# Kernel optimization log

Hardware: AMD Instinct MI355X
Metric: run time of the kernel (lower is better)

Reference implementation:

```python
import jax, jax.numpy as jnp
import numpy as np

D_MODEL = 1024
D_INNER = 2048
D_STATE = 16
D_CONV = 4
DT_RANK = 64
BATCH = 2
SEQ = 1024


def _silu(v):
    return v * jax.nn.sigmoid(v)


def setup_inputs() -> dict:
    key = jax.random.key(0)
    ks = jax.random.split(key, 8)
    s = 0.02
    return {
        "x": jax.random.normal(ks[0], (BATCH, SEQ, D_MODEL), jnp.float32),
        "norm_w": jnp.ones((D_MODEL,), jnp.float32),
        "in_proj_w": (jax.random.normal(ks[1], (2 * D_INNER, D_MODEL), jnp.float32) * s),
        "conv_w": (jax.random.normal(ks[2], (D_INNER, 1, D_CONV), jnp.float32) * s),
        "conv_b": jnp.zeros((D_INNER,), jnp.float32),
        "x_proj_w": (jax.random.normal(ks[3], (DT_RANK + 2 * D_STATE, D_INNER), jnp.float32) * s),
        "dt_proj_w": (jax.random.normal(ks[4], (D_INNER, DT_RANK), jnp.float32) * s),
        "dt_proj_b": jnp.zeros((D_INNER,), jnp.float32),
        "A_log": jnp.log(jnp.broadcast_to(jnp.arange(1, D_STATE + 1, dtype=jnp.float32), (D_INNER, D_STATE))),
        "D": jnp.ones((D_INNER,), jnp.float32),
        "out_proj_w": (jax.random.normal(ks[5], (D_MODEL, D_INNER), jnp.float32) * s),
    }


def reference(x, norm_w, in_proj_w, conv_w, conv_b, x_proj_w, dt_proj_w, dt_proj_b, A_log, D, out_proj_w):
    b, l, d = x.shape
    x_copy = x
    # MambaRMSNorm
    h = x * jax.lax.rsqrt(jnp.mean(x * x, axis=-1, keepdims=True) + 1e-5) * norm_w
    # in_proj -> split into x-path and residual gate
    x_and_res = h @ in_proj_w.T                       # [b, l, 2*d_inner]
    xs, res = jnp.split(x_and_res, 2, axis=-1)
    # causal depthwise conv1d (torch pads d_conv-1 both sides then slices [:l])
    xc = jnp.transpose(xs, (0, 2, 1))                 # [b, d_inner, l]
    xc = jax.lax.conv_general_dilated(
        xc, conv_w, window_strides=(1,), padding=[(D_CONV - 1, 0)],
        feature_group_count=D_INNER, dimension_numbers=("NCH", "OIH", "NCH"))
    xc = xc + conv_b[None, :, None]
    u = _silu(jnp.transpose(xc, (0, 2, 1)))           # [b, l, d_inner]
    # SSM parameters
    A = -jnp.exp(A_log)                               # [d_inner, n]
    x_dbl = u @ x_proj_w.T                            # [b, l, dt_rank + 2n]
    delta, Bm, Cm = jnp.split(x_dbl, [DT_RANK, DT_RANK + D_STATE], axis=-1)
    delta = jax.nn.softplus(delta @ dt_proj_w.T + dt_proj_b)   # [b, l, d_inner]
    deltaA = jnp.exp(jnp.einsum("bld,dn->bldn", delta, A))     # [b, l, d_inner, n]
    deltaB_u = (delta * u)[..., None] * Bm[:, :, None, :]      # [b, l, d_inner, n]

    def step(state, inp):
        dA, dBu, c = inp                               # [b,d,n],[b,d,n],[b,n]
        state = dA * state + dBu
        y = jnp.einsum("bdn,bn->bd", state, c)
        return state, y

    init = jnp.zeros((b, D_INNER, D_STATE), dtype=u.dtype)
    _, ys = jax.lax.scan(
        step, init,
        (jnp.transpose(deltaA, (1, 0, 2, 3)),
         jnp.transpose(deltaB_u, (1, 0, 2, 3)),
         jnp.transpose(Cm, (1, 0, 2))))
    y = jnp.transpose(ys, (1, 0, 2)) + u * D           # [b, l, d_inner]
    y = y * _silu(res)
    return y @ out_proj_w.T + x_copy
```

## Files before the change

### kernel.cpp

```cpp
#include <hip/hip_runtime.h>
#include <hip/hip_bf16.h>
#include <math.h>

constexpr int B_   = 2;
constexpr int L_   = 1024;
constexpr int DM   = 1024;
constexpr int DI   = 2048;
constexpr int NS   = 16;
constexpr int DTR  = 64;
constexpr int TOK  = B_ * L_;
constexpr int NC   = 32;

typedef __attribute__((ext_vector_type(8))) short short8;
typedef __attribute__((ext_vector_type(4))) float f32x4;
using bf16 = __hip_bfloat16;

__device__ __forceinline__ float sigmoidf_(float v) {
    return 1.f / (1.f + __expf(-v));
}
__device__ __forceinline__ float softplusf_(float v) {
    return fmaxf(v, 0.f) + __logf(1.f + __expf(-fabsf(v)));
}

__device__ __forceinline__ f32x4 mfma16(short8 a, short8 b, f32x4 c) {
    return __builtin_amdgcn_mfma_f32_16x16x32_bf16(a, b, c, 0, 0, 0);
}

__global__ __launch_bounds__(256) void k_rmsnorm(
    const float* __restrict__ x, const float* __restrict__ w,
    bf16* __restrict__ hh, bf16* __restrict__ hl)
{
    int row = blockIdx.x;
    const float4* xrp = (const float4*)(x + (size_t)row * DM);
    float4 v = xrp[threadIdx.x];
    float ss = v.x*v.x + v.y*v.y + v.z*v.z + v.w*v.w;
    #pragma unroll
    for (int m = 32; m >= 1; m >>= 1) ss += __shfl_xor(ss, m);
    __shared__ float acc[4];
    int wid = threadIdx.x >> 6, lane = threadIdx.x & 63;
    if (lane == 0) acc[wid] = ss;
    __syncthreads();
    float tot = acc[0] + acc[1] + acc[2] + acc[3];
    float sc = rsqrtf(tot * (1.f / DM) + 1e-5f);
    float4 wv = ((const float4*)w)[threadIdx.x];
    float o[4] = { v.x*sc*wv.x, v.y*sc*wv.y, v.z*sc*wv.z, v.w*sc*wv.w };
    alignas(8) bf16 H[4], Lo[4];
    #pragma unroll
    for (int j = 0; j < 4; ++j) {
        H[j]  = __float2bfloat16(o[j]);
        Lo[j] = __float2bfloat16(o[j] - __bfloat162float(H[j]));
    }
    size_t base = (size_t)row * DM + threadIdx.x * 4;
    *(ushort4*)(hh + base) = *(ushort4*)H;
    *(ushort4*)(hl + base) = *(ushort4*)Lo;
}

__global__ __launch_bounds__(256) void k_split(
    const float* __restrict__ s, bf16* __restrict__ hi, bf16* __restrict__ lo, int n4)
{
    int i = blockIdx.x * 256 + threadIdx.x;
    if (i >= n4) return;
    float4 v = ((const float4*)s)[i];
    float f[4] = { v.x, v.y, v.z, v.w };
    alignas(8) bf16 H[4], Lo[4];
    #pragma unroll
    for (int j = 0; j < 4; ++j) {
        H[j]  = __float2bfloat16(f[j]);
        Lo[j] = __float2bfloat16(f[j] - __bfloat162float(H[j]));
    }
    *(ushort4*)(hi + (size_t)i * 4) = *(ushort4*)H;
    *(ushort4*)(lo + (size_t)i * 4) = *(ushort4*)Lo;
}

__global__ __launch_bounds__(256) void k_split_pad(
    const float* __restrict__ s, bf16* __restrict__ hi, bf16* __restrict__ lo)
{
    int i = blockIdx.x * 256 + threadIdx.x;
    int row = i >> 9;
    float f[4] = {0.f, 0.f, 0.f, 0.f};
    if (row < 96) {
        float4 v = ((const float4*)s)[i];
        f[0] = v.x; f[1] = v.y; f[2] = v.z; f[3] = v.w;
    }
    alignas(8) bf16 H[4], Lo[4];
    #pragma unroll
    for (int j = 0; j < 4; ++j) {
        H[j]  = __float2bfloat16(f[j]);
        Lo[j] = __float2bfloat16(f[j] - __bfloat162float(H[j]));
    }
    *(ushort4*)(hi + (size_t)i * 4) = *(ushort4*)H;
    *(ushort4*)(lo + (size_t)i * 4) = *(ushort4*)Lo;
}

__global__ __launch_bounds__(256) void k_transpose(
    const float* __restrict__ in, float* __restrict__ out)
{
    __shared__ float tile[32][33];
    int tx = threadIdx.x & 31, ty = threadIdx.x >> 5;
    int c0 = blockIdx.x * 32, r0 = blockIdx.y * 32;
    #pragma unroll
    for (int i = 0; i < 4; ++i)
        tile[ty * 4 + i][tx] = in[(size_t)(r0 + ty * 4 + i) * DI + c0 + tx];
    __syncthreads();
    #pragma unroll
    for (int i = 0; i < 4; ++i)
        out[(size_t)(c0 + ty * 4 + i) * TOK + r0 + tx] = tile[tx][ty * 4 + i];
}

__global__ __launch_bounds__(256) void k_tr_bc(
    const float* __restrict__ xdbl, float* __restrict__ bc_t)
{
    int id = blockIdx.x * 256 + threadIdx.x;
    int tok = id & (TOK - 1);
    int j = id >> 11;
    bc_t[(size_t)j * TOK + tok] = xdbl[(size_t)tok * 96 + 64 + j];
}

__device__ __forceinline__ void stage_tile(const bf16* src, int ld, bf16* lds, int lane)
{
    #pragma unroll
    for (int j = 0; j < 8; ++j) {
        int c = (j << 6) + lane;
        int r = c >> 2;
        int g = (c & 3) ^ ((r >> 1) & 3);
        __builtin_amdgcn_global_load_lds(
            (const __attribute__((address_space(1))) unsigned int*)(src + (size_t)r * ld + (g << 3)),
            (__attribute__((address_space(3))) unsigned int*)(lds + (j << 9)),
            16, 0, 0);
    }
}

template<int NA, int EPI>
__global__ __launch_bounds__(256) void k_gemm_bf16(
    const bf16* __restrict__ Ah, const bf16* __restrict__ Al, int lda,
    const bf16* __restrict__ Bh, const bf16* __restrict__ Bl, int ldb,
    float* __restrict__ C, int ldc,
    const float* __restrict__ aux,
    int M, int Nb, int Kc)
{
    __shared__ alignas(1024) bf16 sA[2][NA][128 * 32];
    __shared__ alignas(1024) bf16 sB[2][2][128 * 32];

    int tid = threadIdx.x, lane = tid & 63, wv = tid >> 6;
    int bm0 = blockIdx.y * 128, bn0 = blockIdx.x * 128;
    int kbase = blockIdx.z * Kc;
    int nkt = Kc >> 5;

    const bf16* Abase_h = Ah + (size_t)bm0 * lda + kbase;
    const bf16* Abase_l = (NA == 2) ? (Al + (size_t)bm0 * lda + kbase) : nullptr;
    const bf16* Bbase_h = Bh + (size_t)bn0 * ldb + kbase;
    const bf16* Bbase_l = Bl + (size_t)bn0 * ldb + kbase;

    auto stage_all = [&](int buf, int kt) {
        int k0 = kt << 5;
        if constexpr (NA == 2) {
            if      (wv == 0) stage_tile(Abase_h + k0, lda, &sA[buf][0][0], lane);
            else if (wv == 1) stage_tile(Abase_l + k0, lda, &sA[buf][1][0], lane);
            else if (wv == 2) stage_tile(Bbase_h + k0, ldb, &sB[buf][0][0], lane);
            else              stage_tile(Bbase_l + k0, ldb, &sB[buf][1][0], lane);
        } else {
            if      (wv == 0) stage_tile(Abase_h + k0, lda, &sA[buf][0][0], lane);
            else if (wv == 1) stage_tile(Bbase_h + k0, ldb, &sB[buf][0][0], lane);
            else if (wv == 2) stage_tile(Bbase_l + k0, ldb, &sB[buf][1][0], lane);
        }
    };
    auto frag = [&](const bf16* t, int r, int g) -> short8 {
        int c = (r << 2) + (g ^ ((r >> 1) & 3));
        return *(const short8*)(t + (c << 3));
    };

    int wr = (wv >> 1) << 6;
    int wc = (wv & 1) << 6;
    int fr = lane & 15, g = lane >> 4;

    f32x4 acc[4][4] = {};

    stage_all(0, 0);
    __syncthreads();
    for (int kt = 0; kt < nkt; ++kt) {
        int cur = kt & 1;
        if (kt + 1 < nkt) stage_all(cur ^ 1, kt + 1);
        short8 a0[4], a1[4], b0[4], b1[4];
        #pragma unroll
        for (int m = 0; m < 4; ++m) {
            a0[m] = frag(&sA[cur][0][0], wr + m * 16 + fr, g);
            if constexpr (NA == 2) a1[m] = frag(&sA[cur][NA - 1][0], wr + m * 16 + fr, g);
        }
        #pragma unroll
        for (int n = 0; n < 4; ++n) {
            b0[n] = frag(&sB[cur][0][0], wc + n * 16 + fr, g);
            b1[n] = frag(&sB[cur][1][0], wc + n * 16 + fr, g);
        }
        #pragma unroll
        for (int m = 0; m < 4; ++m)
            #pragma unroll
            for (int n = 0; n < 4; ++n) {
                acc[m][n] = mfma16(a0[m], b0[n], acc[m][n]);
                acc[m][n] = mfma16(a0[m], b1[n], acc[m][n]);
                if constexpr (NA == 2) acc[m][n] = mfma16(a1[m], b0[n], acc[m][n]);
            }
        __syncthreads();
    }

    int rbase = bm0 + wr + (g << 2);
    int cb = bn0 + wc + fr;
    if constexpr (EPI == 4) {
        #pragma unroll
        for (int m = 0; m < 4; ++m)
            #pragma unroll
            for (int n = 0; n < 4; ++n) {
                int col = cb + n * 16;
                float b_ = aux[col];
                float vv[4];
                #pragma unroll
                for (int i = 0; i < 4; ++i)
                    vv[i] = softplusf_(acc[m][n][i] + b_);
                *(float4*)&C[(size_t)col * ldc + rbase + m * 16] = *(float4*)vv;
            }
    } else {
        #pragma unroll
        for (int m = 0; m < 4; ++m)
            #pragma unroll
            for (int i = 0; i < 4; ++i) {
                int row = rbase + m * 16 + i;
                #pragma unroll
                for (int n = 0; n < 4; ++n) {
                    int col = cb + n * 16;
                    float v = acc[m][n][i];
                    if constexpr (EPI == 3) {
                        if (col < Nb) atomicAdd(&C[(size_t)row * ldc + col], v);
                    } else {
                        if constexpr (EPI == 1) v = softplusf_(v + aux[col]);
                        if constexpr (EPI == 2) v += aux[(size_t)row * ldc + col];
                        C[(size_t)row * ldc + col] = v;
                    }
                }
            }
    }
}

__global__ __launch_bounds__(256) void k_conv_silu(
    const float* __restrict__ xr, const float* __restrict__ w,
    const float* __restrict__ bconv, float* __restrict__ u,
    bf16* __restrict__ uh, bf16* __restrict__ ul)
{
    int idx = blockIdx.x * 256 + threadIdx.x;
    int dq = idx & 511;
    int l  = (idx >> 9) & 1023;
    int bb = idx >> 19;
    int dd = dq * 4;

    float4 wrow[4];
    #pragma unroll
    for (int j = 0; j < 4; j++)
        wrow[j] = *(const float4*)&w[(dd + j) * 4];
    float4 bias4 = *(const float4*)&bconv[dd];

    float acc[4] = { bias4.x, bias4.y, bias4.z, bias4.w };
    #pragma unroll
    for (int k = 0; k < 4; k++) {
        int lp = l - 3 + k;
        if (lp >= 0) {
            const float4 xv = *(const float4*)
                &xr[((size_t)(bb * L_ + lp)) * (2 * DI) + dd];
            const float xs_[4] = { xv.x, xv.y, xv.z, xv.w };
            #pragma unroll
            for (int j = 0; j < 4; j++)
                acc[j] = fmaf(xs_[j], ((const float*)&wrow[j])[k], acc[j]);
        }
    }
    float out[4];
    alignas(8) bf16 H[4], Lo[4];
    #pragma unroll
    for (int j = 0; j < 4; j++) {
        out[j] = acc[j] * sigmoidf_(acc[j]);
        H[j]  = __float2bfloat16(out[j]);
        Lo[j] = __float2bfloat16(out[j] - __bfloat162float(H[j]));
    }
    size_t base = ((size_t)(bb * L_ + l)) * DI + dd;
    *(float4*)&u[base] = *(float4*)out;
    *(ushort4*)(uh + base) = *(ushort4*)H;
    *(ushort4*)(ul + base) = *(ushort4*)Lo;
}

__global__ __launch_bounds__(256) void k_scan_part(
    const float* __restrict__ delta_t, const float* __restrict__ u_t,
    const float* __restrict__ bc_t,    const float* __restrict__ A_log,
    float* __restrict__ P, float* __restrict__ S)
{
    int bx = blockIdx.x;
    int c = bx & (NC - 1);
    int rest = bx >> 5;
    int b = rest >> 5;
    int d0 = (rest & 31) << 6;
    int t = threadIdx.x;
    int dl_ = t >> 2, q = t & 3;
    int d = d0 + dl_;

    float A_dn[4];
    #pragma unroll
    for (int j = 0; j < 4; ++j)
        A_dn[j] = -__expf(A_log[d * NS + q * 4 + j]);

    float s[4] = {};
    float dsum = 0.f;
    int tokb = b * L_ + c * (L_ / NC);
    const float* dbase = delta_t + (size_t)d * TOK + tokb;
    const float* ubase = u_t + (size_t)d * TOK + tokb;
    const float* Bbase = bc_t + (size_t)(q * 4) * TOK + tokb;

    for (int g = 0; g < (L_ / NC) / 4; ++g) {
        float4 dl4 = *(const float4*)(dbase + g * 4);
        float4 uu4 = *(const float4*)(ubase + g * 4);
        float Bm_[4][4];
        #pragma unroll
        for (int j = 0; j < 4; ++j) {
            float4 bv = *(const float4*)(Bbase + (size_t)j * TOK + g * 4);
            Bm_[j][0] = bv.x; Bm_[j][1] = bv.y; Bm_[j][2] = bv.z; Bm_[j][3] = bv.w;
        }
        const float dls[4] = {dl4.x, dl4.y, dl4.z, dl4.w};
        const float uus[4] = {uu4.x, uu4.y, uu4.z, uu4.w};
        #pragma unroll
        for (int k = 0; k < 4; ++k) {
            float dlu = dls[k] * uus[k];
            dsum += dls[k];
            #pragma unroll
            for (int j = 0; j < 4; ++j) {
                float e = __expf(dls[k] * A_dn[j]);
                s[j] = fmaf(e, s[j], dlu * Bm_[j][k]);
            }
        }
    }
    float p[4];
    #pragma unroll
    for (int j = 0; j < 4; ++j)
        p[j] = __expf(A_dn[j] * dsum);
    size_t o = (((size_t)(b * NC + c) * DI) + d) * NS + q * 4;
    *(float4*)&P[o] = *(float4*)p;
    *(float4*)&S[o] = *(float4*)s;
}

__global__ __launch_bounds__(256) void k_scan_comb(
    const float* __restrict__ P, float* __restrict__ S)
{
    int idx = blockIdx.x * 256 + threadIdx.x;
    int n = idx & 15;
    int d = (idx >> 4) & (DI - 1);
    int b = idx >> 15;
    float carry = 0.f;
    #pragma unroll
    for (int c = 0; c < NC; ++c) {
        size_t o = (((size_t)(b * NC + c) * DI) + d) * NS + n;
        float Pv = P[o], Sv = S[o];
        S[o] = carry;
        carry = fmaf(Pv, carry, Sv);
    }
}

__global__ __launch_bounds__(256) void k_scan_y(
    const float* __restrict__ delta_t, const float* __restrict__ u_t,
    const float* __restrict__ bc_t,    const float* __restrict__ xr,
    const float* __restrict__ A_log,   const float* __restrict__ Dp,
    const float* __restrict__ init, bf16* __restrict__ y)
{
    int bx = blockIdx.x;
    int c = bx & (NC - 1);
    int rest = bx >> 5;
    int b = rest >> 5;
    int d0 = (rest & 31) << 6;
    int t = threadIdx.x;
    int dl_ = t >> 2, q = t & 3;
    int d = d0 + dl_;

    float A_dn[4];
    #pragma unroll
    for (int j = 0; j < 4; ++j)
        A_dn[j] = -__expf(A_log[d * NS + q * 4 + j]);
    float Dd = Dp[d];

    size_t o = (((size_t)(b * NC + c) * DI) + d) * NS + q * 4;
    float4 s4 = *(const float4*)&init[o];
    float s[4] = {s4.x, s4.y, s4.z, s4.w};

    int tokb = b * L_ + c * (L_ / NC);
    const float* dbase = delta_t + (size_t)d * TOK + tokb;
    const float* ubase = u_t + (size_t)d * TOK + tokb;
    const float* Bbase = bc_t + (size_t)(q * 4) * TOK + tokb;
    const float* Cbase = bc_t + (size_t)(16 + q * 4) * TOK + tokb;

    for (int g = 0; g < (L_ / NC) / 4; ++g) {
        int tok0 = tokb + g * 4;
        float4 dl4 = *(const float4*)(dbase + g * 4);
        float4 uu4 = *(const float4*)(ubase + g * 4);
        float Bm_[4][4], Cm_[4][4];
        #pragma unroll
        for (int j = 0; j < 4; ++j) {
            float4 bv = *(const float4*)(Bbase + (size_t)j * TOK + g * 4);
            float4 cv = *(const float4*)(Cbase + (size_t)j * TOK + g * 4);
            Bm_[j][0] = bv.x; Bm_[j][1] = bv.y; Bm_[j][2] = bv.z; Bm_[j][3] = bv.w;
            Cm_[j][0] = cv.x; Cm_[j][1] = cv.y; Cm_[j][2] = cv.z; Cm_[j][3] = cv.w;
        }
        const float dls[4] = {dl4.x, dl4.y, dl4.z, dl4.w};
        const float uus[4] = {uu4.x, uu4.y, uu4.z, uu4.w};
        float py[4];
        #pragma unroll
        for (int k = 0; k < 4; ++k) {
            float dlu = dls[k] * uus[k];
            float a_ = 0.f;
            #pragma unroll
            for (int j = 0; j < 4; ++j) {
                float e = __expf(dls[k] * A_dn[j]);
                s[j] = fmaf(e, s[j], dlu * Bm_[j][k]);
                a_ = fmaf(s[j], Cm_[j][k], a_);
            }
            py[k] = a_;
        }
        #pragma unroll
        for (int k = 0; k < 4; ++k) {
            py[k] += __shfl_xor(py[k], 1);
            py[k] += __shfl_xor(py[k], 2);
        }
        float py_q = py[0], uu_q = uus[0];
        py_q = (q == 1) ? py[1] : py_q;  uu_q = (q == 1) ? uus[1] : uu_q;
        py_q = (q == 2) ? py[2] : py_q;  uu_q = (q == 2) ? uus[2] : uu_q;
        py_q = (q == 3) ? py[3] : py_q;  uu_q = (q == 3) ? uus[3] : uu_q;
        int tok = tok0 + q;
        float rr = xr[(size_t)tok * (2 * DI) + DI + d];
        float yv = fmaf(uu_q, Dd, py_q) * (rr * sigmoidf_(rr));
        y[(size_t)tok * DI + d] = __float2bfloat16(yv);
    }
}

extern "C" void kernel_launch(void* const* d_in, const int* in_sizes, int n_in,
                              void* d_out, int out_size, void* d_ws, size_t ws_size,
                              hipStream_t stream)
{
    const float* x       = (const float*)d_in[0];
    const float* norm_w  = (const float*)d_in[1];
    const float* in_proj = (const float*)d_in[2];
    const float* conv_w  = (const float*)d_in[3];
    const float* conv_b  = (const float*)d_in[4];
    const float* x_proj  = (const float*)d_in[5];
    const float* dt_w    = (const float*)d_in[6];
    const float* dt_b    = (const float*)d_in[7];
    const float* A_log   = (const float*)d_in[8];
    const float* Dp      = (const float*)d_in[9];
    const float* out_w   = (const float*)d_in[10];
    float* out = (float*)d_out;

    constexpr size_t MB = 1u << 20;
    constexpr size_t KB = 1u << 10;
    char* Wb = (char*)d_ws;
    float* xr      = (float*)(Wb + 0);
    bf16*  h_h     = (bf16*) (Wb + 32 * MB);
    bf16*  h_l     = (bf16*) (Wb + 36 * MB);
    float* u       = (float*)(Wb + 32 * MB);
    float* Pbuf    = (float*)(Wb + 32 * MB);
    bf16*  y_h     = (bf16*) (Wb + 32 * MB);
    float* Sbuf    = (float*)(Wb + 40 * MB);
    bf16*  u_h     = (bf16*) (Wb + 48 * MB);
    bf16*  u_l     = (bf16*) (Wb + 56 * MB);
    float* delta_t = (float*)(Wb + 48 * MB);
    bf16*  wo_h    = (bf16*) (Wb + 48 * MB);
    bf16*  wo_l    = (bf16*) (Wb + 52 * MB);
    bf16*  wi_h    = (bf16*) (Wb + 64 * MB);
    bf16*  wi_l    = (bf16*) (Wb + 72 * MB);
    float* u_t     = (float*)(Wb + 64 * MB);
    float* xdbl    = (float*)(Wb + 80 * MB);
    bf16*  xp_h    = (bf16*) (Wb + 80 * MB + 768 * KB);
    bf16*  xp_l    = (bf16*) (Wb + 81 * MB + 256 * KB);
    float* bc_t    = (float*)(Wb + 81 * MB + 768 * KB);
    bf16*  xdbl_h  = (bf16*) (Wb + 82 * MB);
    bf16*  xdbl_l  = (bf16*) (Wb + 82 * MB + 384 * KB);
    bf16*  dtw_h   = (bf16*) (Wb + 82 * MB + 768 * KB);
    bf16*  dtw_l   = (bf16*) (Wb + 83 * MB);

    k_rmsnorm<<<TOK, 256, 0, stream>>>(x, norm_w, h_h, h_l);
    k_split<<<4096, 256, 0, stream>>>(in_proj, wi_h, wi_l, (2 * DI * DM) / 4);
    k_gemm_bf16<2, 0><<<dim3(32, 16, 1), 256, 0, stream>>>(
        h_h, h_l, DM, wi_h, wi_l, DM, xr, 2 * DI, nullptr, TOK, 2 * DI, DM);
    k_conv_silu<<<4096, 256, 0, stream>>>(xr, conv_w, conv_b, u, u_h, u_l);
    k_split_pad<<<256, 256, 0, stream>>>(x_proj, xp_h, xp_l);
    hipMemsetAsync(xdbl, 0, (size_t)TOK * 96 * sizeof(float), stream);
    k_gemm_bf16<2, 3><<<dim3(1, 16, 8), 256, 0, stream>>>(
        u_h, u_l, DI, xp_h, xp_l, DI, xdbl, 96, nullptr, TOK, 96, DI / 8);
    k_transpose<<<dim3(DI / 32, TOK / 32), 256, 0, stream>>>(u, u_t);
    k_tr_bc<<<256, 256, 0, stream>>>(xdbl, bc_t);
    k_split<<<128, 256, 0, stream>>>(dt_w, dtw_h, dtw_l, (DI * DTR) / 4);
    k_split<<<192, 256, 0, stream>>>(xdbl, xdbl_h, xdbl_l, (TOK * 96) / 4);
    k_gemm_bf16<2, 4><<<dim3(16, 16, 1), 256, 0, stream>>>(
        xdbl_h, xdbl_l, 96, dtw_h, dtw_l, DTR, delta_t, TOK, dt_b, TOK, DI, DTR);
    k_scan_part<<<B_ * NC * (DI / 64), 256, 0, stream>>>(
        delta_t, u_t, bc_t, A_log, Pbuf, Sbuf);
    k_scan_comb<<<256, 256, 0, stream>>>(Pbuf, Sbuf);
    k_scan_y<<<B_ * NC * (DI / 64), 256, 0, stream>>>(
        delta_t, u_t, bc_t, xr, A_log, Dp, Sbuf, y_h);
    k_split<<<2048, 256, 0, stream>>>(out_w, wo_h, wo_l, (DM * DI) / 4);
    k_gemm_bf16<1, 2><<<dim3(8, 16, 1), 256, 0, stream>>>(
        y_h, nullptr, DI, wo_h, wo_l, DI, out, DM, x, TOK, DM, DI);
}
```

Measured before the change: 383.8 us.

## Fuse transposes into conv and xdbl post-pass, split-K x_proj and out_proj GEMMs

The conv+SiLU kernel now handles 8 timesteps per thread, reusing a sliding window of input rows, and writes u directly in transposed layout. This removes the separate fp32 u buffer and its transpose kernel. A new post-pass kernel fuses the bf16 hi/lo split of xdbl with the B/C transpose. The x_proj GEMM's split-K factor rises from 8 to 32. The out_proj GEMM becomes a 4-way split-K with atomic adds into an output pre-filled with the residual by a device copy. These steps aim to cut launches and memory traffic and to raise occupancy on small GEMMs, at the cost of more atomic contention and an extra copy.

```diff
diff --git a/kernel.cpp b/kernel.cpp
--- a/kernel.cpp
+++ b/kernel.cpp
@@ -92,28 +92,17 @@
     *(ushort4*)(lo + (size_t)i * 4) = *(ushort4*)Lo;
 }
 
-__global__ __launch_bounds__(256) void k_transpose(
-    const float* __restrict__ in, float* __restrict__ out)
-{
-    __shared__ float tile[32][33];
-    int tx = threadIdx.x & 31, ty = threadIdx.x >> 5;
-    int c0 = blockIdx.x * 32, r0 = blockIdx.y * 32;
-    #pragma unroll
-    for (int i = 0; i < 4; ++i)
-        tile[ty * 4 + i][tx] = in[(size_t)(r0 + ty * 4 + i) * DI + c0 + tx];
-    __syncthreads();
-    #pragma unroll
-    for (int i = 0; i < 4; ++i)
-        out[(size_t)(c0 + ty * 4 + i) * TOK + r0 + tx] = tile[tx][ty * 4 + i];
-}
-
-__global__ __launch_bounds__(256) void k_tr_bc(
-    const float* __restrict__ xdbl, float* __restrict__ bc_t)
-{
-    int id = blockIdx.x * 256 + threadIdx.x;
-    int tok = id & (TOK - 1);
-    int j = id >> 11;
-    bc_t[(size_t)j * TOK + tok] = xdbl[(size_t)tok * 96 + 64 + j];
+__global__ __launch_bounds__(128) void k_xdbl_post(
+    const float* __restrict__ xdbl, bf16* __restrict__ hi, bf16* __restrict__ lo,
+    float* __restrict__ bc_t)
+{
+    int tok = blockIdx.x, col = threadIdx.x;
+    if (col >= 96) return;
+    float v = xdbl[(size_t)tok * 96 + col];
+    bf16 H = __float2bfloat16(v);
+    hi[(size_t)tok * 96 + col] = H;
+    lo[(size_t)tok * 96 + col] = __float2bfloat16(v - __bfloat162float(H));
+    if (col >= 64) bc_t[(size_t)(col - 64) * TOK + tok] = v;
 }
 
 __device__ __forceinline__ void stage_tile(const bf16* src, int ld, bf16* lds, int lane)
@@ -241,13 +230,14 @@
 
 __global__ __launch_bounds__(256) void k_conv_silu(
     const float* __restrict__ xr, const float* __restrict__ w,
-    const float* __restrict__ bconv, float* __restrict__ u,
-    bf16* __restrict__ uh, bf16* __restrict__ ul)
+    const float* __restrict__ bconv,
+    bf16* __restrict__ uh, bf16* __restrict__ ul, float* __restrict__ u_t)
 {
     int idx = blockIdx.x * 256 + threadIdx.x;
     int dq = idx & 511;
-    int l  = (idx >> 9) & 1023;
-    int bb = idx >> 19;
+    int ts = idx >> 9;
+    int bb = ts >> 7;
+    int t0 = (ts & 127) * 8;
     int dd = dq * 4;
 
     float4 wrow[4];
@@ -255,32 +245,47 @@
     for (int j = 0; j < 4; j++)
         wrow[j] = *(const float4*)&w[(dd + j) * 4];
     float4 bias4 = *(const float4*)&bconv[dd];
-
-    float acc[4] = { bias4.x, bias4.y, bias4.z, bias4.w };
-    #pragma unroll
-    for (int k = 0; k < 4; k++) {
-        int lp = l - 3 + k;
-        if (lp >= 0) {
-            const float4 xv = *(const float4*)
-                &xr[((size_t)(bb * L_ + lp)) * (2 * DI) + dd];
-            const float xs_[4] = { xv.x, xv.y, xv.z, xv.w };
-            #pragma unroll
-            for (int j = 0; j < 4; j++)
-                acc[j] = fmaf(xs_[j], ((const float*)&wrow[j])[k], acc[j]);
-        }
-    }
-    float out[4];
-    alignas(8) bf16 H[4], Lo[4];
-    #pragma unroll
-    for (int j = 0; j < 4; j++) {
-        out[j] = acc[j] * sigmoidf_(acc[j]);
-        H[j]  = __float2bfloat16(out[j]);
-        Lo[j] = __float2bfloat16(out[j] - __bfloat162float(H[j]));
-    }
-    size_t base = ((size_t)(bb * L_ + l)) * DI + dd;
-    *(float4*)&u[base] = *(float4*)out;
-    *(ushort4*)(uh + base) = *(ushort4*)H;
-    *(ushort4*)(ul + base) = *(ushort4*)Lo;
+    const float bias_[4] = { bias4.x, bias4.y, bias4.z, bias4.w };
+
+    auto ldrow = [&](int t) -> float4 {
+        if (t < 0) return make_float4(0.f, 0.f, 0.f, 0.f);
+        return *(const float4*)&xr[((size_t)(bb * L_ + t)) * (2 * DI) + dd];
+    };
+    float4 a = ldrow(t0 - 3), b = ldrow(t0 - 2), c = ldrow(t0 - 1);
+
+    float uout[4][8];
+    #pragma unroll
+    for (int k = 0; k < 8; ++k) {
+        float4 d4 = ldrow(t0 + k);
+        const float as[4] = {a.x, a.y, a.z, a.w};
+        const float bs[4] = {b.x, b.y, b.z, b.w};
+        const float cs[4] = {c.x, c.y, c.z, c.w};
+        const float ds[4] = {d4.x, d4.y, d4.z, d4.w};
+        alignas(8) bf16 H[4], Lo[4];
+        #pragma unroll
+        for (int j = 0; j < 4; ++j) {
+            const float* wj = (const float*)&wrow[j];
+            float acc = bias_[j];
+            acc = fmaf(as[j], wj[0], acc);
+            acc = fmaf(bs[j], wj[1], acc);
+            acc = fmaf(cs[j], wj[2], acc);
+            acc = fmaf(ds[j], wj[3], acc);
+            float o = acc * sigmoidf_(acc);
+            uout[j][k] = o;
+            H[j]  = __float2bfloat16(o);
+            Lo[j] = __float2bfloat16(o - __bfloat162float(H[j]));
+        }
+        size_t base = ((size_t)(bb * L_ + t0 + k)) * DI + dd;
+        *(ushort4*)(uh + base) = *(ushort4*)H;
+        *(ushort4*)(ul + base) = *(ushort4*)Lo;
+        a = b; b = c; c = d4;
+    }
+    #pragma unroll
+    for (int j = 0; j < 4; ++j) {
+        size_t tb = (size_t)(dd + j) * TOK + bb * L_ + t0;
+        *(float4*)&u_t[tb]     = make_float4(uout[j][0], uout[j][1], uout[j][2], uout[j][3]);
+        *(float4*)&u_t[tb + 4] = make_float4(uout[j][4], uout[j][5], uout[j][6], uout[j][7]);
+    }
 }
 
 __global__ __launch_bounds__(256) void k_scan_part(
@@ -454,24 +459,23 @@
     float* xr      = (float*)(Wb + 0);
     bf16*  h_h     = (bf16*) (Wb + 32 * MB);
     bf16*  h_l     = (bf16*) (Wb + 36 * MB);
-    float* u       = (float*)(Wb + 32 * MB);
+    bf16*  u_h     = (bf16*) (Wb + 32 * MB);
+    bf16*  u_l     = (bf16*) (Wb + 40 * MB);
     float* Pbuf    = (float*)(Wb + 32 * MB);
+    float* Sbuf    = (float*)(Wb + 40 * MB);
     bf16*  y_h     = (bf16*) (Wb + 32 * MB);
-    float* Sbuf    = (float*)(Wb + 40 * MB);
-    bf16*  u_h     = (bf16*) (Wb + 48 * MB);
-    bf16*  u_l     = (bf16*) (Wb + 56 * MB);
-    float* delta_t = (float*)(Wb + 48 * MB);
+    float* u_t     = (float*)(Wb + 48 * MB);
     bf16*  wo_h    = (bf16*) (Wb + 48 * MB);
     bf16*  wo_l    = (bf16*) (Wb + 52 * MB);
     bf16*  wi_h    = (bf16*) (Wb + 64 * MB);
     bf16*  wi_l    = (bf16*) (Wb + 72 * MB);
-    float* u_t     = (float*)(Wb + 64 * MB);
+    float* delta_t = (float*)(Wb + 64 * MB);
     float* xdbl    = (float*)(Wb + 80 * MB);
     bf16*  xp_h    = (bf16*) (Wb + 80 * MB + 768 * KB);
     bf16*  xp_l    = (bf16*) (Wb + 81 * MB + 256 * KB);
-    float* bc_t    = (float*)(Wb + 81 * MB + 768 * KB);
-    bf16*  xdbl_h  = (bf16*) (Wb + 82 * MB);
-    bf16*  xdbl_l  = (bf16*) (Wb + 82 * MB + 384 * KB);
+    bf16*  xdbl_h  = (bf16*) (Wb + 81 * MB + 768 * KB);
+    bf16*  xdbl_l  = (bf16*) (Wb + 82 * MB + 128 * KB);
+    float* bc_t    = (float*)(Wb + 82 * MB + 512 * KB);
     bf16*  dtw_h   = (bf16*) (Wb + 82 * MB + 768 * KB);
     bf16*  dtw_l   = (bf16*) (Wb + 83 * MB);
 
@@ -479,15 +483,13 @@
     k_split<<<4096, 256, 0, stream>>>(in_proj, wi_h, wi_l, (2 * DI * DM) / 4);
     k_gemm_bf16<2, 0><<<dim3(32, 16, 1), 256, 0, stream>>>(
         h_h, h_l, DM, wi_h, wi_l, DM, xr, 2 * DI, nullptr, TOK, 2 * DI, DM);
-    k_conv_silu<<<4096, 256, 0, stream>>>(xr, conv_w, conv_b, u, u_h, u_l);
+    k_conv_silu<<<512, 256, 0, stream>>>(xr, conv_w, conv_b, u_h, u_l, u_t);
     k_split_pad<<<256, 256, 0, stream>>>(x_proj, xp_h, xp_l);
     hipMemsetAsync(xdbl, 0, (size_t)TOK * 96 * sizeof(float), stream);
-    k_gemm_bf16<2, 3><<<dim3(1, 16, 8), 256, 0, stream>>>(
-        u_h, u_l, DI, xp_h, xp_l, DI, xdbl, 96, nullptr, TOK, 96, DI / 8);
-    k_transpose<<<dim3(DI / 32, TOK / 32), 256, 0, stream>>>(u, u_t);
-    k_tr_bc<<<256, 256, 0, stream>>>(xdbl, bc_t);
+    k_gemm_bf16<2, 3><<<dim3(1, 16, 32), 256, 0, stream>>>(
+        u_h, u_l, DI, xp_h, xp_l, DI, xdbl, 96, nullptr, TOK, 96, DI / 32);
+    k_xdbl_post<<<TOK, 128, 0, stream>>>(xdbl, xdbl_h, xdbl_l, bc_t);
     k_split<<<128, 256, 0, stream>>>(dt_w, dtw_h, dtw_l, (DI * DTR) / 4);
-    k_split<<<192, 256, 0, stream>>>(xdbl, xdbl_h, xdbl_l, (TOK * 96) / 4);
     k_gemm_bf16<2, 4><<<dim3(16, 16, 1), 256, 0, stream>>>(
         xdbl_h, xdbl_l, 96, dtw_h, dtw_l, DTR, delta_t, TOK, dt_b, TOK, DI, DTR);
     k_scan_part<<<B_ * NC * (DI / 64), 256, 0, stream>>>(
@@ -496,6 +498,8 @@
     k_scan_y<<<B_ * NC * (DI / 64), 256, 0, stream>>>(
         delta_t, u_t, bc_t, xr, A_log, Dp, Sbuf, y_h);
     k_split<<<2048, 256, 0, stream>>>(out_w, wo_h, wo_l, (DM * DI) / 4);
-    k_gemm_bf16<1, 2><<<dim3(8, 16, 1), 256, 0, stream>>>(
-        y_h, nullptr, DI, wo_h, wo_l, DI, out, DM, x, TOK, DM, DI);
-}
+    hipMemcpyAsync(out, x, (size_t)TOK * DM * sizeof(float),
+                   hipMemcpyDeviceToDevice, stream);
+    k_gemm_bf16<1, 3><<<dim3(8, 16, 4), 256, 0, stream>>>(
+        y_h, nullptr, DI, wo_h, wo_l, DI, out, DM, nullptr, TOK, DM, DI / 4);
+}
```

New measurement: 368.2 us. 4.1% less time.
